# Performance work log

Hardware: AMD Instinct MI355X
Metric: run time of the kernel (lower is better)

Reference implementation:

```python
import jax, jax.numpy as jnp
import numpy as np

PE_DIM = 40  # pe_dim; gaussian PE scale factor = pe_dim // 2


def _batched_linear(x, wb):
    # x: [B, N, D], wb: [B, D+1, H] (last row is bias)
    return jnp.einsum('bnd,bdh->bnh', x, wb[:, :-1, :]) + wb[:, -1:, :]


def setup_inputs() -> dict:
    key = jax.random.key(0)
    ks = jax.random.split(key, 8)
    B, N = 16, 16384
    H = 256
    pe_out = 3 * PE_DIM  # 120
    s = 0.05  # keep ReLU-chain activations bounded
    return {
        'x': jax.random.normal(ks[0], (B, N, 3), dtype=jnp.float32),
        'wb0': jax.random.normal(ks[1], (B, pe_out + 1, H), dtype=jnp.float32) * s,
        'wb1': jax.random.normal(ks[2], (B, H + 1, H), dtype=jnp.float32) * s,
        'wb2': jax.random.normal(ks[3], (B, H + 1, H), dtype=jnp.float32) * s,
        'wb3': jax.random.normal(ks[4], (B, H + 1, H), dtype=jnp.float32) * s,
        'wb4': jax.random.normal(ks[5], (B, H + 1, H), dtype=jnp.float32) * s,
        'wb_out': jax.random.normal(ks[6], (B, H + 1, 1), dtype=jnp.float32) * s,
        'rand_freqs': jax.random.normal(ks[7], (3 * (PE_DIM // 2), 3), dtype=jnp.float32),  # feat_sigma=1
    }


def reference(x, wb0, wb1, wb2, wb3, wb4, wb_out, rand_freqs):
    # Gaussian positional encoding: k = x . (rand_freqs * pe_dim//2)
    k = jnp.einsum('bnd,fd->bnf', x, rand_freqs * (PE_DIM // 2))  # [B,N,60]
    h = jnp.concatenate([jnp.sin(k), jnp.cos(k)], axis=-1)        # [B,N,120]
    for wb in (wb0, wb1, wb2, wb3, wb4):
        h = jax.nn.relu(_batched_linear(h, wb))
    out = _batched_linear(h, wb_out)  # [B,N,1]
    return out
```

## Files before the change

### kernel.cpp

```cpp
#include <hip/hip_runtime.h>
#include <hip/hip_bf16.h>


#define H 256
#define MT 64
#define PE_NF 60

typedef __attribute__((ext_vector_type(8))) short s16x8;
typedef __attribute__((ext_vector_type(4))) float f32x4;

static __device__ __forceinline__ unsigned short f2bf(float v) {
  unsigned int u = __float_as_uint(v);
  return (unsigned short)((u + 0x7FFFu + ((u >> 16) & 1u)) >> 16);
}
static __device__ __forceinline__ int hswz(int row, int chunk) {
  return (chunk & ~7) | ((chunk ^ row) & 7);
}

static __device__ __forceinline__ void bar_raw() {
  asm volatile("s_barrier" ::: "memory");
}
static __device__ __forceinline__ void bar_lgkm() {
  asm volatile("s_waitcnt lgkmcnt(0)\n\ts_barrier" ::: "memory");
}

__global__ __launch_bounds__(256) void prep_weights(
    const float* __restrict__ wb0, const float* __restrict__ wb1,
    const float* __restrict__ wb2, const float* __restrict__ wb3,
    const float* __restrict__ wb4,
    unsigned short* __restrict__ w0p, unsigned short* __restrict__ w14p,
    float* __restrict__ biases) {
  int z = blockIdx.z;
  int li = z >> 4, b = z & 15;
  int k0 = blockIdx.x * 32;
  int n0 = blockIdx.y * 32;
  int Ks;
  const float* src;
  unsigned short* dst;
  if (li == 0) {
    Ks = 120;
    if (k0 >= 128) return;
    src = wb0 + (size_t)b * 121 * H;
    dst = w0p + (size_t)b * 32768;
  } else {
    Ks = 256;
    const float* srcs[4] = {wb1, wb2, wb3, wb4};
    src = srcs[li - 1] + (size_t)b * 257 * H;
    dst = w14p + ((size_t)(li - 1) * 16 + b) * 65536;
  }
  __shared__ float tile[32][33];
  int t = threadIdx.x;
  int tx = t & 31, ty = t >> 5;
#pragma unroll
  for (int i = 0; i < 4; ++i) {
    int k = k0 + ty + i * 8;
    tile[ty + i * 8][tx] = (k < Ks) ? src[(size_t)k * H + n0 + tx] : 0.f;
  }
  if (k0 == 0 && ty == 0)
    biases[((size_t)li * 16 + b) * H + n0 + tx] = src[(size_t)Ks * H + n0 + tx];
  __syncthreads();
  if (t < 128) {
    int nn = t & 31, kg = t >> 5;
    int n = n0 + nn;
    int kt = k0 >> 5;
    union { unsigned short us[8]; s16x8 v; } pk;
#pragma unroll
    for (int j = 0; j < 8; ++j) pk.us[j] = f2bf(tile[kg * 8 + j][nn]);
    *(s16x8*)&dst[(size_t)(kt * 16 + (n >> 4)) * 512 + (kg * 16 + (n & 15)) * 8] = pk.v;
  }
}

template <int NKT, bool LAST>
static __device__ __forceinline__ void mlp_layer(
    const char* fpb, const char* fpn, const float* __restrict__ bl,
    unsigned short* __restrict__ h_s,
    const int rlane, const int kgrp, const int wc, const int l,
    s16x8 (&wf)[2][4], const float* wout_r, float* psum) {
  static_assert((NKT & 1) == 0, "ping-pong parity needs even NKT");
  f32x4 acc[4][4];
#pragma unroll
  for (int ct = 0; ct < 4; ++ct) {
    f32x4 bini = *(const f32x4*)(bl + wc * 64 + ct * 16 + kgrp * 4);
#pragma unroll
    for (int rt = 0; rt < 4; ++rt) acc[rt][ct] = bini;
  }

  const char* hb = (const char*)h_s;
  const unsigned be = rlane * 512 + hswz(rlane, kgrp) * 16;
  const unsigned bo = rlane * 512 + hswz(rlane, 4 + kgrp) * 16;

  s16x8 af[2][4];
#pragma unroll
  for (int rt = 0; rt < 4; ++rt)
    af[0][rt] = *(const s16x8*)(hb + be + rt * 8192);

#pragma unroll
  for (int kt = 0; kt < NKT; ++kt) {
    if (kt + 1 < NKT) {
      fpb += 16384;
#pragma unroll
      for (int c = 0; c < 4; ++c)
        wf[(kt + 1) & 1][c] = *(const s16x8*)(fpb + c * 1024);
      const unsigned base = ((kt + 1) & 1) ? bo : be;
      const unsigned off = ((kt + 1) >> 1) * 128;
#pragma unroll
      for (int rt = 0; rt < 4; ++rt)
        af[(kt + 1) & 1][rt] = *(const s16x8*)(hb + base + off + rt * 8192);
    } else if (!LAST) {
#pragma unroll
      for (int c = 0; c < 4; ++c)
        wf[0][c] = *(const s16x8*)(fpn + c * 1024);
    }
    __builtin_amdgcn_s_setprio(1);
#pragma unroll
    for (int rt = 0; rt < 4; ++rt)
#pragma unroll
      for (int ct = 0; ct < 4; ++ct)
        acc[rt][ct] = __builtin_amdgcn_mfma_f32_16x16x32_bf16(
            wf[kt & 1][ct], af[kt & 1][rt], acc[rt][ct], 0, 0, 0);
    __builtin_amdgcn_s_setprio(0);
  }

  if constexpr (LAST) {
    float p[4];
#pragma unroll
    for (int rt = 0; rt < 4; ++rt) {
      float s = 0.f;
#pragma unroll
      for (int ct = 0; ct < 4; ++ct)
#pragma unroll
        for (int g = 0; g < 4; ++g)
          s += fmaxf(acc[rt][ct][g], 0.f) * wout_r[ct * 4 + g];
      s += __shfl_xor(s, 16);
      s += __shfl_xor(s, 32);
      p[rt] = s;
    }
    if (l < 16) {
#pragma unroll
      for (int rt = 0; rt < 4; ++rt)
        psum[wc * 64 + rt * 16 + l] = p[rt];
    }
  } else {
    bar_raw();
    const int sub = (kgrp & 1) * 4;
    const int cbase = wc * 8 + (kgrp >> 1);
#pragma unroll
    for (int rt = 0; rt < 4; ++rt) {
      const int m = rt * 16 + rlane;
      const int rowb = m * 256;
#pragma unroll
      for (int ct = 0; ct < 4; ++ct) {
        const int cs = hswz(m, cbase + ct * 2);
        float v0 = fmaxf(acc[rt][ct][0], 0.f);
        float v1 = fmaxf(acc[rt][ct][1], 0.f);
        float v2 = fmaxf(acc[rt][ct][2], 0.f);
        float v3 = fmaxf(acc[rt][ct][3], 0.f);
        union { __hip_bfloat162 h2[2]; uint2 u; } pk;
        pk.h2[0] = __float22bfloat162_rn(float2{v0, v1});
        pk.h2[1] = __float22bfloat162_rn(float2{v2, v3});
        *(uint2*)&h_s[rowb + cs * 8 + sub] = pk.u;
      }
    }
    bar_lgkm();
  }
}

__global__ __launch_bounds__(256, 3) void hyponerf_main(
    const float* __restrict__ x, const float* __restrict__ rfreq,
    const float* __restrict__ wbout,
    const unsigned short* __restrict__ w0p, const unsigned short* __restrict__ w14p,
    const float* __restrict__ biases, float* __restrict__ out) {
  __shared__ __align__(16) unsigned short h_s[MT * 256];
  __shared__ float fr_s[PE_NF * 3];
  __shared__ float x_s[MT * 3];
  __shared__ float psum[4 * 64];

  int bid = blockIdx.x;
  int logical = (bid & 7) * 512 + (bid >> 3);
  int b  = logical >> 8;
  int mt = logical & 255;

  int t = threadIdx.x;
  int wc = t >> 6, l = t & 63;
  int rlane = l & 15;
  int kgrp  = l >> 4;

  const size_t lane_off = ((size_t)wc * 4 * 512 + l * 8) * 2;
  const char* f0 = (const char*)(w0p + (size_t)b * 32768) + lane_off;
  const char* f1 = (const char*)(w14p + (size_t)(0 * 16 + b) * 65536) + lane_off;
  const char* f2 = (const char*)(w14p + (size_t)(1 * 16 + b) * 65536) + lane_off;
  const char* f3 = (const char*)(w14p + (size_t)(2 * 16 + b) * 65536) + lane_off;
  const char* f4 = (const char*)(w14p + (size_t)(3 * 16 + b) * 65536) + lane_off;

  s16x8 wf[2][4];
#pragma unroll
  for (int c = 0; c < 4; ++c) wf[0][c] = *(const s16x8*)(f0 + c * 1024);

  float wout_r[16];
  {
    const float* wob = wbout + (size_t)b * (H + 1) + wc * 64 + kgrp * 4;
#pragma unroll
    for (int ct = 0; ct < 4; ++ct)
#pragma unroll
      for (int g = 0; g < 4; ++g) wout_r[ct * 4 + g] = wob[ct * 16 + g];
  }
  const float wout_bias = wbout[(size_t)b * (H + 1) + H];

  const float* xg = x + ((size_t)b * 16384 + (size_t)mt * MT) * 3;
  for (int i = t; i < MT * 3; i += 256) x_s[i] = xg[i];
  for (int i = t; i < PE_NF * 3; i += 256) fr_s[i] = rfreq[i] * 20.0f;
  bar_lgkm();

  {
    int r = t >> 2;
    int q = t & 3;
    float x0 = x_s[r * 3 + 0], x1 = x_s[r * 3 + 1], x2 = x_s[r * 3 + 2];
    int rowb = r * 256;
#pragma unroll
    for (int cc = 0; cc < 4; ++cc) {
      int ch = q * 4 + cc;
      union { unsigned short us[8]; s16x8 v; } pk;
#pragma unroll
      for (int j = 0; j < 8; ++j) {
        int n = ch * 8 + j;
        float v = 0.f;
        if (n < 60) {
          float kv = x0 * fr_s[n * 3] + x1 * fr_s[n * 3 + 1] + x2 * fr_s[n * 3 + 2];
          v = __sinf(kv);
        } else if (n < 120) {
          int f = n - 60;
          float kv = x0 * fr_s[f * 3] + x1 * fr_s[f * 3 + 1] + x2 * fr_s[f * 3 + 2];
          v = __cosf(kv);
        }
        pk.us[j] = f2bf(v);
      }
      *(s16x8*)&h_s[rowb + hswz(r, ch) * 8] = pk.v;
    }
  }
  bar_lgkm();

  const float* bb = biases + (size_t)b * H;
  mlp_layer<4, false>(f0, f1, bb + 0 * 16 * H, h_s, rlane, kgrp, wc, l, wf,
                      wout_r, psum);
  mlp_layer<8, false>(f1, f2, bb + 1 * 16 * H, h_s, rlane, kgrp, wc, l, wf,
                      wout_r, psum);
  mlp_layer<8, false>(f2, f3, bb + 2 * 16 * H, h_s, rlane, kgrp, wc, l, wf,
                      wout_r, psum);
  mlp_layer<8, false>(f3, f4, bb + 3 * 16 * H, h_s, rlane, kgrp, wc, l, wf,
                      wout_r, psum);
  mlp_layer<8, true >(f4, f4, bb + 4 * 16 * H, h_s, rlane, kgrp, wc, l, wf,
                      wout_r, psum);

  bar_lgkm();
  if (t < MT) {
    float s = psum[t] + psum[64 + t] + psum[128 + t] + psum[192 + t];
    out[(size_t)b * 16384 + (size_t)mt * MT + t] = s + wout_bias;
  }
}

extern "C" void kernel_launch(void* const* d_in, const int* in_sizes, int n_in,
                              void* d_out, int out_size, void* d_ws, size_t ws_size,
                              hipStream_t stream) {
  const float* x     = (const float*)d_in[0];
  const float* wb0   = (const float*)d_in[1];
  const float* wb1   = (const float*)d_in[2];
  const float* wb2   = (const float*)d_in[3];
  const float* wb3   = (const float*)d_in[4];
  const float* wb4   = (const float*)d_in[5];
  const float* wbout = (const float*)d_in[6];
  const float* rfreq = (const float*)d_in[7];
  float* out = (float*)d_out;

  char* ws = (char*)d_ws;
  unsigned short* w0p  = (unsigned short*)ws;
  unsigned short* w14p = (unsigned short*)(ws + (size_t)16 * 32768 * 2);
  float* biases = (float*)(ws + (size_t)16 * 32768 * 2
                              + (size_t)64 * 65536 * 2);

  prep_weights<<<dim3(8, 8, 80), 256, 0, stream>>>(wb0, wb1, wb2, wb3, wb4,
                                                   w0p, w14p, biases);
  hyponerf_main<<<dim3(4096), 256, 0, stream>>>(x, rfreq, wbout, w0p, w14p,
                                                biases, out);
}
```

Baseline: 165.7 us.

## Switch MLP layers from 16x16x32 to 32x32x16 bf16 MFMA with repacked weights

Replaces the 4x4 grid of 16x16x32 MFMA tiles per wave with a 2x2 grid of 32x32x16 MFMAs. The weight prep kernel repacks fragments to the 32x32 operand layout, and the LDS activation reads and swizzled writebacks are remapped to match. The larger MFMA issues fewer instructions and reads fewer operand registers per FLOP, and it shrinks the final-layer cross-lane reduction to one shuffle. The output-layer weights move from registers to shared memory to lower register pressure, at the cost of extra LDS reads in the last layer.

New measurement: 177.0 us. +6.8%, slower.

```diff
diff --git a/kernel.cpp b/kernel.cpp
--- a/kernel.cpp
+++ b/kernel.cpp
@@ -8,6 +8,7 @@
 
 typedef __attribute__((ext_vector_type(8))) short s16x8;
 typedef __attribute__((ext_vector_type(4))) float f32x4;
+typedef __attribute__((ext_vector_type(16))) float f32x16;
 
 static __device__ __forceinline__ unsigned short f2bf(float v) {
   unsigned int u = __float_as_uint(v);
@@ -61,38 +62,52 @@
   __syncthreads();
   if (t < 128) {
     int nn = t & 31, kg = t >> 5;
-    int n = n0 + nn;
-    int kt = k0 >> 5;
+    int kt = k0 >> 5, nt = n0 >> 5;
+    int kh = kg >> 1;
+    int lane = nn + (kg & 1) * 32;
+    int frag = (kt * 8 + nt) * 2 + kh;
     union { unsigned short us[8]; s16x8 v; } pk;
 #pragma unroll
     for (int j = 0; j < 8; ++j) pk.us[j] = f2bf(tile[kg * 8 + j][nn]);
-    *(s16x8*)&dst[(size_t)(kt * 16 + (n >> 4)) * 512 + (kg * 16 + (n & 15)) * 8] = pk.v;
+    *(s16x8*)&dst[(size_t)frag * 512 + lane * 8] = pk.v;
   }
 }
 
 template <int NKT, bool LAST>
 static __device__ __forceinline__ void mlp_layer(
     const char* fpb, const char* fpn, const float* __restrict__ bl,
-    unsigned short* __restrict__ h_s,
-    const int rlane, const int kgrp, const int wc, const int l,
-    s16x8 (&wf)[2][4], const float* wout_r, float* psum) {
+    unsigned short* __restrict__ h_s, const float* __restrict__ wout_s,
+    const int m32, const int hi, const int wc, const int l,
+    s16x8 (&wf)[2][4], float* psum) {
   static_assert((NKT & 1) == 0, "ping-pong parity needs even NKT");
-  f32x4 acc[4][4];
-#pragma unroll
-  for (int ct = 0; ct < 4; ++ct) {
-    f32x4 bini = *(const f32x4*)(bl + wc * 64 + ct * 16 + kgrp * 4);
-#pragma unroll
-    for (int rt = 0; rt < 4; ++rt) acc[rt][ct] = bini;
-  }
+
+  f32x16 acc[2][2];
+#pragma unroll
+  for (int ntl = 0; ntl < 2; ++ntl)
+#pragma unroll
+    for (int q = 0; q < 4; ++q) {
+      f32x4 bq = *(const f32x4*)(bl + wc * 64 + ntl * 32 + q * 8 + hi * 4);
+#pragma unroll
+      for (int s = 0; s < 4; ++s) {
+        acc[0][ntl][q * 4 + s] = bq[s];
+        acc[1][ntl][q * 4 + s] = bq[s];
+      }
+    }
 
   const char* hb = (const char*)h_s;
-  const unsigned be = rlane * 512 + hswz(rlane, kgrp) * 16;
-  const unsigned bo = rlane * 512 + hswz(rlane, 4 + kgrp) * 16;
+  unsigned ab[2][2];
+#pragma unroll
+  for (int p = 0; p < 2; ++p)
+#pragma unroll
+    for (int kh = 0; kh < 2; ++kh)
+      ab[p][kh] = m32 * 512 + (((4 * p + 2 * kh + hi) ^ (m32 & 7)) & 7) * 16;
 
   s16x8 af[2][4];
 #pragma unroll
-  for (int rt = 0; rt < 4; ++rt)
-    af[0][rt] = *(const s16x8*)(hb + be + rt * 8192);
+  for (int mt = 0; mt < 2; ++mt)
+#pragma unroll
+    for (int kh = 0; kh < 2; ++kh)
+      af[0][mt * 2 + kh] = *(const s16x8*)(hb + ab[0][kh] + mt * 16384);
 
 #pragma unroll
   for (int kt = 0; kt < NKT; ++kt) {
@@ -101,11 +116,14 @@
 #pragma unroll
       for (int c = 0; c < 4; ++c)
         wf[(kt + 1) & 1][c] = *(const s16x8*)(fpb + c * 1024);
-      const unsigned base = ((kt + 1) & 1) ? bo : be;
+      const int p1 = (kt + 1) & 1;
       const unsigned off = ((kt + 1) >> 1) * 128;
 #pragma unroll
-      for (int rt = 0; rt < 4; ++rt)
-        af[(kt + 1) & 1][rt] = *(const s16x8*)(hb + base + off + rt * 8192);
+      for (int mt = 0; mt < 2; ++mt)
+#pragma unroll
+        for (int kh = 0; kh < 2; ++kh)
+          af[p1][mt * 2 + kh] =
+              *(const s16x8*)(hb + ab[p1][kh] + off + mt * 16384);
     } else if (!LAST) {
 #pragma unroll
       for (int c = 0; c < 4; ++c)
@@ -113,53 +131,58 @@
     }
     __builtin_amdgcn_s_setprio(1);
 #pragma unroll
-    for (int rt = 0; rt < 4; ++rt)
-#pragma unroll
-      for (int ct = 0; ct < 4; ++ct)
-        acc[rt][ct] = __builtin_amdgcn_mfma_f32_16x16x32_bf16(
-            wf[kt & 1][ct], af[kt & 1][rt], acc[rt][ct], 0, 0, 0);
+    for (int mt = 0; mt < 2; ++mt)
+#pragma unroll
+      for (int ntl = 0; ntl < 2; ++ntl)
+#pragma unroll
+        for (int kh = 0; kh < 2; ++kh)
+          acc[mt][ntl] = __builtin_amdgcn_mfma_f32_32x32x16_bf16(
+              wf[kt & 1][ntl * 2 + kh], af[kt & 1][mt * 2 + kh],
+              acc[mt][ntl], 0, 0, 0);
     __builtin_amdgcn_s_setprio(0);
   }
 
   if constexpr (LAST) {
-    float p[4];
-#pragma unroll
-    for (int rt = 0; rt < 4; ++rt) {
+    float p[2];
+#pragma unroll
+    for (int mt = 0; mt < 2; ++mt) {
       float s = 0.f;
 #pragma unroll
-      for (int ct = 0; ct < 4; ++ct)
-#pragma unroll
-        for (int g = 0; g < 4; ++g)
-          s += fmaxf(acc[rt][ct][g], 0.f) * wout_r[ct * 4 + g];
-      s += __shfl_xor(s, 16);
+      for (int ntl = 0; ntl < 2; ++ntl)
+#pragma unroll
+        for (int q = 0; q < 4; ++q) {
+          f32x4 wv = *(const f32x4*)(wout_s + wc * 64 + ntl * 32 + q * 8 + hi * 4);
+#pragma unroll
+          for (int s2 = 0; s2 < 4; ++s2)
+            s += fmaxf(acc[mt][ntl][q * 4 + s2], 0.f) * wv[s2];
+        }
       s += __shfl_xor(s, 32);
-      p[rt] = s;
-    }
-    if (l < 16) {
-#pragma unroll
-      for (int rt = 0; rt < 4; ++rt)
-        psum[wc * 64 + rt * 16 + l] = p[rt];
+      p[mt] = s;
+    }
+    if (l < 32) {
+      psum[wc * 64 + l]      = p[0];
+      psum[wc * 64 + 32 + l] = p[1];
     }
   } else {
     bar_raw();
-    const int sub = (kgrp & 1) * 4;
-    const int cbase = wc * 8 + (kgrp >> 1);
-#pragma unroll
-    for (int rt = 0; rt < 4; ++rt) {
-      const int m = rt * 16 + rlane;
+#pragma unroll
+    for (int mt = 0; mt < 2; ++mt) {
+      const int m = mt * 32 + m32;
       const int rowb = m * 256;
 #pragma unroll
-      for (int ct = 0; ct < 4; ++ct) {
-        const int cs = hswz(m, cbase + ct * 2);
-        float v0 = fmaxf(acc[rt][ct][0], 0.f);
-        float v1 = fmaxf(acc[rt][ct][1], 0.f);
-        float v2 = fmaxf(acc[rt][ct][2], 0.f);
-        float v3 = fmaxf(acc[rt][ct][3], 0.f);
-        union { __hip_bfloat162 h2[2]; uint2 u; } pk;
-        pk.h2[0] = __float22bfloat162_rn(float2{v0, v1});
-        pk.h2[1] = __float22bfloat162_rn(float2{v2, v3});
-        *(uint2*)&h_s[rowb + cs * 8 + sub] = pk.u;
-      }
+      for (int ntl = 0; ntl < 2; ++ntl)
+#pragma unroll
+        for (int q = 0; q < 4; ++q) {
+          const int cs = hswz(m, wc * 8 + ntl * 4 + q);
+          float v0 = fmaxf(acc[mt][ntl][q * 4 + 0], 0.f);
+          float v1 = fmaxf(acc[mt][ntl][q * 4 + 1], 0.f);
+          float v2 = fmaxf(acc[mt][ntl][q * 4 + 2], 0.f);
+          float v3 = fmaxf(acc[mt][ntl][q * 4 + 3], 0.f);
+          union { __hip_bfloat162 h2[2]; uint2 u; } pk;
+          pk.h2[0] = __float22bfloat162_rn(float2{v0, v1});
+          pk.h2[1] = __float22bfloat162_rn(float2{v2, v3});
+          *(uint2*)&h_s[rowb + cs * 8 + hi * 4] = pk.u;
+        }
     }
     bar_lgkm();
   }
@@ -173,6 +196,7 @@
   __shared__ __align__(16) unsigned short h_s[MT * 256];
   __shared__ float fr_s[PE_NF * 3];
   __shared__ float x_s[MT * 3];
+  __shared__ float wout_s[H + 1];
   __shared__ float psum[4 * 64];
 
   int bid = blockIdx.x;
@@ -182,10 +206,10 @@
 
   int t = threadIdx.x;
   int wc = t >> 6, l = t & 63;
-  int rlane = l & 15;
-  int kgrp  = l >> 4;
-
-  const size_t lane_off = ((size_t)wc * 4 * 512 + l * 8) * 2;
+  int m32 = l & 31;
+  int hi  = l >> 5;
+
+  const size_t lane_off = (size_t)wc * 4096 + (size_t)l * 16;
   const char* f0 = (const char*)(w0p + (size_t)b * 32768) + lane_off;
   const char* f1 = (const char*)(w14p + (size_t)(0 * 16 + b) * 65536) + lane_off;
   const char* f2 = (const char*)(w14p + (size_t)(1 * 16 + b) * 65536) + lane_off;
@@ -196,19 +220,10 @@
 #pragma unroll
   for (int c = 0; c < 4; ++c) wf[0][c] = *(const s16x8*)(f0 + c * 1024);
 
-  float wout_r[16];
-  {
-    const float* wob = wbout + (size_t)b * (H + 1) + wc * 64 + kgrp * 4;
-#pragma unroll
-    for (int ct = 0; ct < 4; ++ct)
-#pragma unroll
-      for (int g = 0; g < 4; ++g) wout_r[ct * 4 + g] = wob[ct * 16 + g];
-  }
-  const float wout_bias = wbout[(size_t)b * (H + 1) + H];
-
   const float* xg = x + ((size_t)b * 16384 + (size_t)mt * MT) * 3;
   for (int i = t; i < MT * 3; i += 256) x_s[i] = xg[i];
   for (int i = t; i < PE_NF * 3; i += 256) fr_s[i] = rfreq[i] * 20.0f;
+  for (int i = t; i < H + 1; i += 256) wout_s[i] = wbout[(size_t)b * (H + 1) + i];
   bar_lgkm();
 
   {
@@ -240,21 +255,21 @@
   bar_lgkm();
 
   const float* bb = biases + (size_t)b * H;
-  mlp_layer<4, false>(f0, f1, bb + 0 * 16 * H, h_s, rlane, kgrp, wc, l, wf,
-                      wout_r, psum);
-  mlp_layer<8, false>(f1, f2, bb + 1 * 16 * H, h_s, rlane, kgrp, wc, l, wf,
-                      wout_r, psum);
-  mlp_layer<8, false>(f2, f3, bb + 2 * 16 * H, h_s, rlane, kgrp, wc, l, wf,
-                      wout_r, psum);
-  mlp_layer<8, false>(f3, f4, bb + 3 * 16 * H, h_s, rlane, kgrp, wc, l, wf,
-                      wout_r, psum);
-  mlp_layer<8, true >(f4, f4, bb + 4 * 16 * H, h_s, rlane, kgrp, wc, l, wf,
-                      wout_r, psum);
+  mlp_layer<4, false>(f0, f1, bb + 0 * 16 * H, h_s, wout_s, m32, hi, wc, l,
+                      wf, psum);
+  mlp_layer<8, false>(f1, f2, bb + 1 * 16 * H, h_s, wout_s, m32, hi, wc, l,
+                      wf, psum);
+  mlp_layer<8, false>(f2, f3, bb + 2 * 16 * H, h_s, wout_s, m32, hi, wc, l,
+                      wf, psum);
+  mlp_layer<8, false>(f3, f4, bb + 3 * 16 * H, h_s, wout_s, m32, hi, wc, l,
+                      wf, psum);
+  mlp_layer<8, true >(f4, f4, bb + 4 * 16 * H, h_s, wout_s, m32, hi, wc, l,
+                      wf, psum);
 
   bar_lgkm();
   if (t < MT) {
     float s = psum[t] + psum[64 + t] + psum[128 + t] + psum[192 + t];
-    out[(size_t)b * 16384 + (size_t)mt * MT + t] = s + wout_bias;
+    out[(size_t)b * 16384 + (size_t)mt * MT + t] = s + wout_s[H];
   }
 }
 
```

## Retile MLP waves as 2x2 grid with 32 rows by 128 columns each

Applied to the files above, without the earlier changes.

Changes the per-wave tile from 64 rows by 64 columns to 32 rows by 128 columns, arranged as a 2x2 wave grid. Each wave now loads half as many activation fragments from LDS per k-step but twice as many weight fragments from global/L2. It splits weight loading into an A half (prefetched) and a B half (loaded inside the loop) to overlap with MFMAs. The output weights move from registers to shared memory to cut register pressure. This trades less LDS traffic for more global weight traffic and shallower weight prefetch.

Result: slower. 190.0 us (+14.7%).

```diff
diff --git a/kernel.cpp b/kernel.cpp
--- a/kernel.cpp
+++ b/kernel.cpp
@@ -73,83 +73,100 @@
 template <int NKT, bool LAST>
 static __device__ __forceinline__ void mlp_layer(
     const char* fpb, const char* fpn, const float* __restrict__ bl,
-    unsigned short* __restrict__ h_s,
-    const int rlane, const int kgrp, const int wc, const int l,
-    s16x8 (&wf)[2][4], const float* wout_r, float* psum) {
-  static_assert((NKT & 1) == 0, "ping-pong parity needs even NKT");
-  f32x4 acc[4][4];
-#pragma unroll
-  for (int ct = 0; ct < 4; ++ct) {
-    f32x4 bini = *(const f32x4*)(bl + wc * 64 + ct * 16 + kgrp * 4);
-#pragma unroll
-    for (int rt = 0; rt < 4; ++rt) acc[rt][ct] = bini;
-  }
+    unsigned short* __restrict__ h_s, const float* __restrict__ wout_s,
+    const int rlane, const int kgrp, const int wr, const int wc, const int l,
+    s16x8 (&wfA)[4], float* psum) {
+  static_assert((NKT & 1) == 0, "parity needs even NKT");
+  f32x4 acc[2][8];
+#pragma unroll
+  for (int ct = 0; ct < 8; ++ct) {
+    f32x4 bini = *(const f32x4*)(bl + wc * 128 + ct * 16 + kgrp * 4);
+    acc[0][ct] = bini;
+    acc[1][ct] = bini;
+  }
+
+  const char* fpb2 = fpb + 4096;
 
   const char* hb = (const char*)h_s;
-  const unsigned be = rlane * 512 + hswz(rlane, kgrp) * 16;
-  const unsigned bo = rlane * 512 + hswz(rlane, 4 + kgrp) * 16;
-
-  s16x8 af[2][4];
-#pragma unroll
-  for (int rt = 0; rt < 4; ++rt)
-    af[0][rt] = *(const s16x8*)(hb + be + rt * 8192);
+  const unsigned be = wr * 16384 + rlane * 512 + hswz(rlane, kgrp) * 16;
+  const unsigned bo = wr * 16384 + rlane * 512 + hswz(rlane, 4 + kgrp) * 16;
+
+  s16x8 af[2][2];
+  af[0][0] = *(const s16x8*)(hb + be);
+  af[0][1] = *(const s16x8*)(hb + be + 8192);
 
 #pragma unroll
   for (int kt = 0; kt < NKT; ++kt) {
+    s16x8 wfB[4];
+#pragma unroll
+    for (int c = 0; c < 4; ++c)
+      wfB[c] = *(const s16x8*)(fpb2 + c * 1024);
+    fpb2 += 16384;
+    __builtin_amdgcn_s_setprio(1);
+#pragma unroll
+    for (int rt = 0; rt < 2; ++rt)
+#pragma unroll
+      for (int c = 0; c < 4; ++c)
+        acc[rt][c] = __builtin_amdgcn_mfma_f32_16x16x32_bf16(
+            wfA[c], af[kt & 1][rt], acc[rt][c], 0, 0, 0);
+    __builtin_amdgcn_s_setprio(0);
+
     if (kt + 1 < NKT) {
       fpb += 16384;
 #pragma unroll
       for (int c = 0; c < 4; ++c)
-        wf[(kt + 1) & 1][c] = *(const s16x8*)(fpb + c * 1024);
-      const unsigned base = ((kt + 1) & 1) ? bo : be;
+        wfA[c] = *(const s16x8*)(fpb + c * 1024);
+      const int p1 = (kt + 1) & 1;
+      const unsigned base = p1 ? bo : be;
       const unsigned off = ((kt + 1) >> 1) * 128;
-#pragma unroll
-      for (int rt = 0; rt < 4; ++rt)
-        af[(kt + 1) & 1][rt] = *(const s16x8*)(hb + base + off + rt * 8192);
+      af[p1][0] = *(const s16x8*)(hb + base + off);
+      af[p1][1] = *(const s16x8*)(hb + base + off + 8192);
     } else if (!LAST) {
 #pragma unroll
       for (int c = 0; c < 4; ++c)
-        wf[0][c] = *(const s16x8*)(fpn + c * 1024);
+        wfA[c] = *(const s16x8*)(fpn + c * 1024);
     }
     __builtin_amdgcn_s_setprio(1);
 #pragma unroll
-    for (int rt = 0; rt < 4; ++rt)
-#pragma unroll
-      for (int ct = 0; ct < 4; ++ct)
-        acc[rt][ct] = __builtin_amdgcn_mfma_f32_16x16x32_bf16(
-            wf[kt & 1][ct], af[kt & 1][rt], acc[rt][ct], 0, 0, 0);
+    for (int rt = 0; rt < 2; ++rt)
+#pragma unroll
+      for (int c = 0; c < 4; ++c)
+        acc[rt][c + 4] = __builtin_amdgcn_mfma_f32_16x16x32_bf16(
+            wfB[c], af[kt & 1][rt], acc[rt][c + 4], 0, 0, 0);
     __builtin_amdgcn_s_setprio(0);
   }
 
   if constexpr (LAST) {
-    float p[4];
-#pragma unroll
-    for (int rt = 0; rt < 4; ++rt) {
+    float p[2];
+#pragma unroll
+    for (int rt = 0; rt < 2; ++rt) {
       float s = 0.f;
 #pragma unroll
-      for (int ct = 0; ct < 4; ++ct)
+      for (int ct = 0; ct < 8; ++ct) {
+        f32x4 wv = *(const f32x4*)(wout_s + wc * 128 + ct * 16 + kgrp * 4);
 #pragma unroll
         for (int g = 0; g < 4; ++g)
-          s += fmaxf(acc[rt][ct][g], 0.f) * wout_r[ct * 4 + g];
+          s += fmaxf(acc[rt][ct][g], 0.f) * wv[g];
+      }
       s += __shfl_xor(s, 16);
       s += __shfl_xor(s, 32);
       p[rt] = s;
     }
     if (l < 16) {
-#pragma unroll
-      for (int rt = 0; rt < 4; ++rt)
-        psum[wc * 64 + rt * 16 + l] = p[rt];
+      const int wbase = (wr * 2 + wc) * 32;
+      psum[wbase + l]      = p[0];
+      psum[wbase + 16 + l] = p[1];
     }
   } else {
     bar_raw();
     const int sub = (kgrp & 1) * 4;
-    const int cbase = wc * 8 + (kgrp >> 1);
-#pragma unroll
-    for (int rt = 0; rt < 4; ++rt) {
-      const int m = rt * 16 + rlane;
+    const int cbase = wc * 16 + (kgrp >> 1);
+#pragma unroll
+    for (int rt = 0; rt < 2; ++rt) {
+      const int m = wr * 32 + rt * 16 + rlane;
       const int rowb = m * 256;
 #pragma unroll
-      for (int ct = 0; ct < 4; ++ct) {
+      for (int ct = 0; ct < 8; ++ct) {
         const int cs = hswz(m, cbase + ct * 2);
         float v0 = fmaxf(acc[rt][ct][0], 0.f);
         float v1 = fmaxf(acc[rt][ct][1], 0.f);
@@ -173,7 +190,8 @@
   __shared__ __align__(16) unsigned short h_s[MT * 256];
   __shared__ float fr_s[PE_NF * 3];
   __shared__ float x_s[MT * 3];
-  __shared__ float psum[4 * 64];
+  __shared__ float wout_s[H + 1];
+  __shared__ float psum[4 * 32];
 
   int bid = blockIdx.x;
   int logical = (bid & 7) * 512 + (bid >> 3);
@@ -181,34 +199,26 @@
   int mt = logical & 255;
 
   int t = threadIdx.x;
-  int wc = t >> 6, l = t & 63;
+  int w = t >> 6, l = t & 63;
   int rlane = l & 15;
   int kgrp  = l >> 4;
-
-  const size_t lane_off = ((size_t)wc * 4 * 512 + l * 8) * 2;
+  int wr = w >> 1, wc = w & 1;
+
+  const size_t lane_off = (size_t)wc * 8192 + (size_t)l * 16;
   const char* f0 = (const char*)(w0p + (size_t)b * 32768) + lane_off;
   const char* f1 = (const char*)(w14p + (size_t)(0 * 16 + b) * 65536) + lane_off;
   const char* f2 = (const char*)(w14p + (size_t)(1 * 16 + b) * 65536) + lane_off;
   const char* f3 = (const char*)(w14p + (size_t)(2 * 16 + b) * 65536) + lane_off;
   const char* f4 = (const char*)(w14p + (size_t)(3 * 16 + b) * 65536) + lane_off;
 
-  s16x8 wf[2][4];
-#pragma unroll
-  for (int c = 0; c < 4; ++c) wf[0][c] = *(const s16x8*)(f0 + c * 1024);
-
-  float wout_r[16];
-  {
-    const float* wob = wbout + (size_t)b * (H + 1) + wc * 64 + kgrp * 4;
-#pragma unroll
-    for (int ct = 0; ct < 4; ++ct)
-#pragma unroll
-      for (int g = 0; g < 4; ++g) wout_r[ct * 4 + g] = wob[ct * 16 + g];
-  }
-  const float wout_bias = wbout[(size_t)b * (H + 1) + H];
+  s16x8 wfA[4];
+#pragma unroll
+  for (int c = 0; c < 4; ++c) wfA[c] = *(const s16x8*)(f0 + c * 1024);
 
   const float* xg = x + ((size_t)b * 16384 + (size_t)mt * MT) * 3;
   for (int i = t; i < MT * 3; i += 256) x_s[i] = xg[i];
   for (int i = t; i < PE_NF * 3; i += 256) fr_s[i] = rfreq[i] * 20.0f;
+  for (int i = t; i < H + 1; i += 256) wout_s[i] = wbout[(size_t)b * (H + 1) + i];
   bar_lgkm();
 
   {
@@ -240,21 +250,22 @@
   bar_lgkm();
 
   const float* bb = biases + (size_t)b * H;
-  mlp_layer<4, false>(f0, f1, bb + 0 * 16 * H, h_s, rlane, kgrp, wc, l, wf,
-                      wout_r, psum);
-  mlp_layer<8, false>(f1, f2, bb + 1 * 16 * H, h_s, rlane, kgrp, wc, l, wf,
-                      wout_r, psum);
-  mlp_layer<8, false>(f2, f3, bb + 2 * 16 * H, h_s, rlane, kgrp, wc, l, wf,
-                      wout_r, psum);
-  mlp_layer<8, false>(f3, f4, bb + 3 * 16 * H, h_s, rlane, kgrp, wc, l, wf,
-                      wout_r, psum);
-  mlp_layer<8, true >(f4, f4, bb + 4 * 16 * H, h_s, rlane, kgrp, wc, l, wf,
-                      wout_r, psum);
+  mlp_layer<4, false>(f0, f1, bb + 0 * 16 * H, h_s, wout_s, rlane, kgrp,
+                      wr, wc, l, wfA, psum);
+  mlp_layer<8, false>(f1, f2, bb + 1 * 16 * H, h_s, wout_s, rlane, kgrp,
+                      wr, wc, l, wfA, psum);
+  mlp_layer<8, false>(f2, f3, bb + 2 * 16 * H, h_s, wout_s, rlane, kgrp,
+                      wr, wc, l, wfA, psum);
+  mlp_layer<8, false>(f3, f4, bb + 3 * 16 * H, h_s, wout_s, rlane, kgrp,
+                      wr, wc, l, wfA, psum);
+  mlp_layer<8, true >(f4, f4, bb + 4 * 16 * H, h_s, wout_s, rlane, kgrp,
+                      wr, wc, l, wfA, psum);
 
   bar_lgkm();
   if (t < MT) {
-    float s = psum[t] + psum[64 + t] + psum[128 + t] + psum[192 + t];
-    out[(size_t)b * 16384 + (size_t)mt * MT + t] = s + wout_bias;
+    int wrg = t >> 5, ri = t & 31;
+    float s = psum[(wrg * 2) * 32 + ri] + psum[(wrg * 2 + 1) * 32 + ri];
+    out[(size_t)b * 16384 + (size_t)mt * MT + t] = s + wout_s[H];
   }
 }
 
```

## Cut register pressure for 4 waves/SIMD: drop A-fragment prefetch, move wout to LDS

Applied to the files above, without the earlier changes.

The LDS activation fragments are no longer double-buffered across k-steps. They are now loaded at the start of each k-step, while the weight fragments are still prefetched one step ahead through a single running pointer. Per-batch packed weights are made contiguous, and the output-layer weights are staged in shared memory instead of 16 registers. The launch bound is raised from 3 to 4 blocks per CU, trading LDS-latency hiding for higher occupancy.

After: 174.8 us. 1.05x slower.

```diff
diff --git a/kernel.cpp b/kernel.cpp
--- a/kernel.cpp
+++ b/kernel.cpp
@@ -8,6 +8,9 @@
 
 typedef __attribute__((ext_vector_type(8))) short s16x8;
 typedef __attribute__((ext_vector_type(4))) float f32x4;
+
+#define BATCH_BYTES (size_t)589824
+#define BATCH_ELEMS (size_t)294912
 
 static __device__ __forceinline__ unsigned short f2bf(float v) {
   unsigned int u = __float_as_uint(v);
@@ -28,8 +31,7 @@
     const float* __restrict__ wb0, const float* __restrict__ wb1,
     const float* __restrict__ wb2, const float* __restrict__ wb3,
     const float* __restrict__ wb4,
-    unsigned short* __restrict__ w0p, unsigned short* __restrict__ w14p,
-    float* __restrict__ biases) {
+    unsigned short* __restrict__ wpk, float* __restrict__ biases) {
   int z = blockIdx.z;
   int li = z >> 4, b = z & 15;
   int k0 = blockIdx.x * 32;
@@ -41,12 +43,12 @@
     Ks = 120;
     if (k0 >= 128) return;
     src = wb0 + (size_t)b * 121 * H;
-    dst = w0p + (size_t)b * 32768;
+    dst = wpk + b * BATCH_ELEMS;
   } else {
     Ks = 256;
     const float* srcs[4] = {wb1, wb2, wb3, wb4};
     src = srcs[li - 1] + (size_t)b * 257 * H;
-    dst = w14p + ((size_t)(li - 1) * 16 + b) * 65536;
+    dst = wpk + b * BATCH_ELEMS + 32768 + (size_t)(li - 1) * 65536;
   }
   __shared__ float tile[32][33];
   int t = threadIdx.x;
@@ -72,11 +74,11 @@
 
 template <int NKT, bool LAST>
 static __device__ __forceinline__ void mlp_layer(
-    const char* fpb, const char* fpn, const float* __restrict__ bl,
-    unsigned short* __restrict__ h_s,
+    const char*& fp, const float* __restrict__ bl,
+    unsigned short* __restrict__ h_s, const float* __restrict__ wout_s,
     const int rlane, const int kgrp, const int wc, const int l,
-    s16x8 (&wf)[2][4], const float* wout_r, float* psum) {
-  static_assert((NKT & 1) == 0, "ping-pong parity needs even NKT");
+    s16x8 (&wf)[2][4], float* psum) {
+  static_assert((NKT & 1) == 0, "parity needs even NKT");
   f32x4 acc[4][4];
 #pragma unroll
   for (int ct = 0; ct < 4; ++ct) {
@@ -89,27 +91,19 @@
   const unsigned be = rlane * 512 + hswz(rlane, kgrp) * 16;
   const unsigned bo = rlane * 512 + hswz(rlane, 4 + kgrp) * 16;
 
-  s16x8 af[2][4];
-#pragma unroll
-  for (int rt = 0; rt < 4; ++rt)
-    af[0][rt] = *(const s16x8*)(hb + be + rt * 8192);
-
 #pragma unroll
   for (int kt = 0; kt < NKT; ++kt) {
-    if (kt + 1 < NKT) {
-      fpb += 16384;
+    s16x8 af[4];
+    const unsigned base = ((kt & 1) ? bo : be) + (kt >> 1) * 128;
+#pragma unroll
+    for (int rt = 0; rt < 4; ++rt)
+      af[rt] = *(const s16x8*)(hb + base + rt * 8192);
+
+    if (!(LAST && kt == NKT - 1)) {
 #pragma unroll
       for (int c = 0; c < 4; ++c)
-        wf[(kt + 1) & 1][c] = *(const s16x8*)(fpb + c * 1024);
-      const unsigned base = ((kt + 1) & 1) ? bo : be;
-      const unsigned off = ((kt + 1) >> 1) * 128;
-#pragma unroll
-      for (int rt = 0; rt < 4; ++rt)
-        af[(kt + 1) & 1][rt] = *(const s16x8*)(hb + base + off + rt * 8192);
-    } else if (!LAST) {
-#pragma unroll
-      for (int c = 0; c < 4; ++c)
-        wf[0][c] = *(const s16x8*)(fpn + c * 1024);
+        wf[(kt + 1) & 1][c] = *(const s16x8*)(fp + c * 1024);
+      fp += 16384;
     }
     __builtin_amdgcn_s_setprio(1);
 #pragma unroll
@@ -117,7 +111,7 @@
 #pragma unroll
       for (int ct = 0; ct < 4; ++ct)
         acc[rt][ct] = __builtin_amdgcn_mfma_f32_16x16x32_bf16(
-            wf[kt & 1][ct], af[kt & 1][rt], acc[rt][ct], 0, 0, 0);
+            wf[kt & 1][ct], af[rt], acc[rt][ct], 0, 0, 0);
     __builtin_amdgcn_s_setprio(0);
   }
 
@@ -127,10 +121,12 @@
     for (int rt = 0; rt < 4; ++rt) {
       float s = 0.f;
 #pragma unroll
-      for (int ct = 0; ct < 4; ++ct)
+      for (int ct = 0; ct < 4; ++ct) {
+        f32x4 wv = *(const f32x4*)(wout_s + wc * 64 + ct * 16 + kgrp * 4);
 #pragma unroll
         for (int g = 0; g < 4; ++g)
-          s += fmaxf(acc[rt][ct][g], 0.f) * wout_r[ct * 4 + g];
+          s += fmaxf(acc[rt][ct][g], 0.f) * wv[g];
+      }
       s += __shfl_xor(s, 16);
       s += __shfl_xor(s, 32);
       p[rt] = s;
@@ -165,14 +161,14 @@
   }
 }
 
-__global__ __launch_bounds__(256, 3) void hyponerf_main(
+__global__ __launch_bounds__(256, 4) void hyponerf_main(
     const float* __restrict__ x, const float* __restrict__ rfreq,
-    const float* __restrict__ wbout,
-    const unsigned short* __restrict__ w0p, const unsigned short* __restrict__ w14p,
+    const float* __restrict__ wbout, const unsigned short* __restrict__ wpk,
     const float* __restrict__ biases, float* __restrict__ out) {
   __shared__ __align__(16) unsigned short h_s[MT * 256];
   __shared__ float fr_s[PE_NF * 3];
   __shared__ float x_s[MT * 3];
+  __shared__ float wout_s[H + 1];
   __shared__ float psum[4 * 64];
 
   int bid = blockIdx.x;
@@ -185,30 +181,18 @@
   int rlane = l & 15;
   int kgrp  = l >> 4;
 
-  const size_t lane_off = ((size_t)wc * 4 * 512 + l * 8) * 2;
-  const char* f0 = (const char*)(w0p + (size_t)b * 32768) + lane_off;
-  const char* f1 = (const char*)(w14p + (size_t)(0 * 16 + b) * 65536) + lane_off;
-  const char* f2 = (const char*)(w14p + (size_t)(1 * 16 + b) * 65536) + lane_off;
-  const char* f3 = (const char*)(w14p + (size_t)(2 * 16 + b) * 65536) + lane_off;
-  const char* f4 = (const char*)(w14p + (size_t)(3 * 16 + b) * 65536) + lane_off;
+  const char* fp = (const char*)wpk + b * BATCH_BYTES
+                 + (size_t)wc * 4096 + (size_t)l * 16;
 
   s16x8 wf[2][4];
 #pragma unroll
-  for (int c = 0; c < 4; ++c) wf[0][c] = *(const s16x8*)(f0 + c * 1024);
-
-  float wout_r[16];
-  {
-    const float* wob = wbout + (size_t)b * (H + 1) + wc * 64 + kgrp * 4;
-#pragma unroll
-    for (int ct = 0; ct < 4; ++ct)
-#pragma unroll
-      for (int g = 0; g < 4; ++g) wout_r[ct * 4 + g] = wob[ct * 16 + g];
-  }
-  const float wout_bias = wbout[(size_t)b * (H + 1) + H];
+  for (int c = 0; c < 4; ++c) wf[0][c] = *(const s16x8*)(fp + c * 1024);
+  fp += 16384;
 
   const float* xg = x + ((size_t)b * 16384 + (size_t)mt * MT) * 3;
   for (int i = t; i < MT * 3; i += 256) x_s[i] = xg[i];
   for (int i = t; i < PE_NF * 3; i += 256) fr_s[i] = rfreq[i] * 20.0f;
+  for (int i = t; i < H + 1; i += 256) wout_s[i] = wbout[(size_t)b * (H + 1) + i];
   bar_lgkm();
 
   {
@@ -240,21 +224,21 @@
   bar_lgkm();
 
   const float* bb = biases + (size_t)b * H;
-  mlp_layer<4, false>(f0, f1, bb + 0 * 16 * H, h_s, rlane, kgrp, wc, l, wf,
-                      wout_r, psum);
-  mlp_layer<8, false>(f1, f2, bb + 1 * 16 * H, h_s, rlane, kgrp, wc, l, wf,
-                      wout_r, psum);
-  mlp_layer<8, false>(f2, f3, bb + 2 * 16 * H, h_s, rlane, kgrp, wc, l, wf,
-                      wout_r, psum);
-  mlp_layer<8, false>(f3, f4, bb + 3 * 16 * H, h_s, rlane, kgrp, wc, l, wf,
-                      wout_r, psum);
-  mlp_layer<8, true >(f4, f4, bb + 4 * 16 * H, h_s, rlane, kgrp, wc, l, wf,
-                      wout_r, psum);
+  mlp_layer<4, false>(fp, bb + 0 * 16 * H, h_s, wout_s, rlane, kgrp, wc, l,
+                      wf, psum);
+  mlp_layer<8, false>(fp, bb + 1 * 16 * H, h_s, wout_s, rlane, kgrp, wc, l,
+                      wf, psum);
+  mlp_layer<8, false>(fp, bb + 2 * 16 * H, h_s, wout_s, rlane, kgrp, wc, l,
+                      wf, psum);
+  mlp_layer<8, false>(fp, bb + 3 * 16 * H, h_s, wout_s, rlane, kgrp, wc, l,
+                      wf, psum);
+  mlp_layer<8, true >(fp, bb + 4 * 16 * H, h_s, wout_s, rlane, kgrp, wc, l,
+                      wf, psum);
 
   bar_lgkm();
   if (t < MT) {
     float s = psum[t] + psum[64 + t] + psum[128 + t] + psum[192 + t];
-    out[(size_t)b * 16384 + (size_t)mt * MT + t] = s + wout_bias;
+    out[(size_t)b * 16384 + (size_t)mt * MT + t] = s + wout_s[H];
   }
 }
 
@@ -272,13 +256,11 @@
   float* out = (float*)d_out;
 
   char* ws = (char*)d_ws;
-  unsigned short* w0p  = (unsigned short*)ws;
-  unsigned short* w14p = (unsigned short*)(ws + (size_t)16 * 32768 * 2);
-  float* biases = (float*)(ws + (size_t)16 * 32768 * 2
-                              + (size_t)64 * 65536 * 2);
+  unsigned short* wpk = (unsigned short*)ws;
+  float* biases = (float*)(ws + 16 * BATCH_BYTES);
 
   prep_weights<<<dim3(8, 8, 80), 256, 0, stream>>>(wb0, wb1, wb2, wb3, wb4,
-                                                   w0p, w14p, biases);
-  hyponerf_main<<<dim3(4096), 256, 0, stream>>>(x, rfreq, wbout, w0p, w14p,
+                                                   wpk, biases);
+  hyponerf_main<<<dim3(4096), 256, 0, stream>>>(x, rfreq, wbout, wpk,
                                                 biases, out);
 }
```
